# Optimization experiments

Measured on AMD Instinct MI355X. Metric: run time of the kernel, lower is better.

## Reference

```python
import jax, jax.numpy as jnp
import numpy as np
import math

B, C, IMG, P = 256, 3, 32, 4
D, H = 256, 8
HD = D // H
T = (IMG // P) ** 2          # 64 patches
T1 = T + 1                   # +cls token
MLP_H = 2048
HEAD_H = T * D // 2          # 8192
NUM_CLASSES = 10
PATCH_DIM = C * P * P


def _pe(t1, d):
    pos = jnp.arange(t1, dtype=jnp.float32)[:, None]
    div = jnp.exp(jnp.arange(0, d, 2, dtype=jnp.float32) * (-math.log(10000.0) / d))
    s = jnp.sin(pos * div)   # [T1, d/2]
    c = jnp.cos(pos * div)
    return jnp.stack([s, c], axis=-1).reshape(t1, d)  # interleave: even=sin, odd=cos


def _ln2d(x, w, b, eps=1e-5):
    # LayerNorm over last two dims [T1, D] with affine params of shape [T1, D]
    mu = jnp.mean(x, axis=(-2, -1), keepdims=True)
    var = jnp.mean((x - mu) ** 2, axis=(-2, -1), keepdims=True)
    return (x - mu) * jax.lax.rsqrt(var + eps) * w + b


def setup_inputs() -> dict:
    key = jax.random.key(0)
    ks = jax.random.split(key, 16)
    s = 0.02
    inp = {
        "x": jax.random.normal(ks[0], (B, C, IMG, IMG), dtype=jnp.float32),
        "cls_token": jax.random.normal(ks[1], (1, 1, D), dtype=jnp.float32),
        "Wp": jax.random.normal(ks[2], (PATCH_DIM, D), dtype=jnp.float32) * s,
        "bp": jnp.zeros((D,), jnp.float32),
        # 2 transformer blocks, params stacked on leading axis
        "qkv_w": jax.random.normal(ks[3], (2, D, 3 * D), dtype=jnp.float32) * s,
        "qkv_b": jnp.zeros((2, 3 * D), jnp.float32),
        "ln_w": jnp.ones((2, T1, D), jnp.float32),
        "ln_b": jnp.zeros((2, T1, D), jnp.float32),
        "mlp1_w": jax.random.normal(ks[4], (2, D, MLP_H), dtype=jnp.float32) * s,
        "mlp1_b": jnp.zeros((2, MLP_H), jnp.float32),
        "mlp2_w": jax.random.normal(ks[5], (2, MLP_H, D), dtype=jnp.float32) * s,
        "mlp2_b": jnp.zeros((2, D), jnp.float32),
        "head1_w": jax.random.normal(ks[6], (T1 * D, HEAD_H), dtype=jnp.float32) * s,
        "head1_b": jnp.zeros((HEAD_H,), jnp.float32),
        "head2_w": jax.random.normal(ks[7], (HEAD_H, NUM_CLASSES), dtype=jnp.float32) * s,
        "head2_b": jnp.zeros((NUM_CLASSES,), jnp.float32),
    }
    return inp


def reference(x, cls_token, Wp, bp, qkv_w, qkv_b, ln_w, ln_b,
              mlp1_w, mlp1_b, mlp2_w, mlp2_b, head1_w, head1_b, head2_w, head2_b):
    b = x.shape[0]
    n = IMG // P
    # patchify: [B,C,n,P,n,P] -> [B,n,n,C,P,P] -> [B, T, C*P*P]  (C-major per patch)
    patches = x.reshape(b, C, n, P, n, P).transpose(0, 2, 4, 1, 3, 5).reshape(b, T, PATCH_DIM)
    out = patches @ Wp + bp                                     # [B, T, D]
    cls = jnp.broadcast_to(cls_token, (b, 1, D))
    out = jnp.concatenate([cls, out], axis=1)                   # [B, T1, D]
    out = out + _pe(T1, D)[None]

    scale = 1.0 / math.sqrt(HD)
    for i in range(2):  # dropout is eval-mode identity
        h = _ln2d(out, ln_w[i], ln_b[i])
        qkv = (h @ qkv_w[i] + qkv_b[i]).reshape(b, T1, H, 3, HD)
        q, k, v = qkv[..., 0, :], qkv[..., 1, :], qkv[..., 2, :]   # [B,S,H,hd]
        scores = jnp.einsum('bqhd,bkhd->bhqk', q, k) * scale
        a = jax.nn.softmax(scores, axis=-1)
        attn = jnp.einsum('bhqk,bkhd->bqhd', a, v).reshape(b, T1, D)
        r = attn + out
        h2 = _ln2d(r, ln_w[i], ln_b[i])                          # same LN reused
        m = jax.nn.relu(h2 @ mlp1_w[i] + mlp1_b[i])
        out = (m @ mlp2_w[i] + mlp2_b[i]) + r

    flat = out.reshape(b, T1 * D)
    hidden = jax.nn.silu(flat @ head1_w + head1_b)
    return hidden @ head2_w + head2_b                            # [B, 10] logits
```

## Files before the change

kernel.cpp:

```cpp
#include <hip/hip_runtime.h>
#include <hip/hip_fp16.h>
#include <math.h>
#include <stdint.h>

#define B_ 256
#define C_ 3
#define IMG_ 32
#define D_ 256
#define H_ 8
#define HD_ 32
#define T1_ 65
#define MLP_H_ 2048
#define HEAD_H_ 8192
#define NCLS 10
#define PDIM 48
#define M_ROWS (B_*T1_)

typedef _Float16 f16;
typedef _Float16 f16x8 __attribute__((ext_vector_type(8)));
typedef _Float16 f16x4 __attribute__((ext_vector_type(4)));
typedef float f32x4 __attribute__((ext_vector_type(4)));

typedef const void __attribute__((address_space(1))) glob_cv;
typedef void __attribute__((address_space(3))) lds_v;

__device__ __forceinline__ void async16(const void* g, void* l) {
    __builtin_amdgcn_global_load_lds((glob_cv*)g, (lds_v*)l, 16, 0, 0);
}

__global__ __launch_bounds__(256) void patch_embed_kernel(
        const float* __restrict__ x, const float* __restrict__ cls,
        const float* __restrict__ Wp, const float* __restrict__ bp,
        float* __restrict__ out) {
    int bt = blockIdx.x;
    int b = bt / T1_;
    int t = bt % T1_;
    int d = threadIdx.x;
    int i2 = d & ~1;
    float div = expf((float)i2 * (-9.210340371976184f / 256.0f));
    float ang = (float)t * div;
    float pe = (d & 1) ? cosf(ang) : sinf(ang);

    __shared__ float patch[PDIM];
    if (t > 0) {
        int p = t - 1;
        int py = p >> 3, px = p & 7;
        if (threadIdx.x < PDIM) {
            int j = threadIdx.x;
            int c = j >> 4, r = j & 15;
            int iy = r >> 2, ix = r & 3;
            patch[j] = x[((b * C_ + c) * IMG_ + py * 4 + iy) * IMG_ + px * 4 + ix];
        }
    }
    __syncthreads();
    float acc;
    if (t == 0) {
        acc = cls[d];
    } else {
        acc = bp[d];
        #pragma unroll
        for (int j = 0; j < PDIM; ++j) acc += patch[j] * Wp[j * D_ + d];
    }
    out[(size_t)bt * D_ + d] = acc + pe;
}

__global__ __launch_bounds__(256) void ln_kernel(
        const float* __restrict__ xin, const float* __restrict__ w,
        const float* __restrict__ bb, f16* __restrict__ hout) {
    int b = blockIdx.x;
    const float* xb = xin + (size_t)b * (T1_ * D_);
    float s = 0.f, s2 = 0.f;
    for (int i = threadIdx.x; i < T1_ * D_; i += 256) {
        float v = xb[i]; s += v; s2 += v * v;
    }
    #pragma unroll
    for (int o = 32; o > 0; o >>= 1) { s += __shfl_down(s, o); s2 += __shfl_down(s2, o); }
    __shared__ float rs[4], rs2[4];
    __shared__ float mu_s, rstd_s;
    int wid = threadIdx.x >> 6;
    if ((threadIdx.x & 63) == 0) { rs[wid] = s; rs2[wid] = s2; }
    __syncthreads();
    if (threadIdx.x == 0) {
        float S = rs[0] + rs[1] + rs[2] + rs[3];
        float S2 = rs2[0] + rs2[1] + rs2[2] + rs2[3];
        const float inv_n = 1.0f / (float)(T1_ * D_);
        float mu = S * inv_n;
        float var = S2 * inv_n - mu * mu;
        mu_s = mu; rstd_s = rsqrtf(var + 1e-5f);
    }
    __syncthreads();
    float mu = mu_s, rstd = rstd_s;
    f16* hb = hout + (size_t)b * (T1_ * D_);
    for (int i = threadIdx.x; i < T1_ * D_; i += 256) {
        float v = (xb[i] - mu) * rstd * w[i] + bb[i];
        hb[i] = (f16)v;
    }
}

__global__ __launch_bounds__(256) void transpose_cvt(
        const float* __restrict__ W, f16* __restrict__ Wt, int K, int N) {
    __shared__ float L[32][33];
    int n0 = blockIdx.x * 32, k0 = blockIdx.y * 32;
    int t = threadIdx.x;
    int r = t >> 3, c4 = (t & 7) * 4;
    const float4 v = *(const float4*)(W + (size_t)(k0 + r) * N + n0 + c4);
    L[r][c4] = v.x; L[r][c4 + 1] = v.y; L[r][c4 + 2] = v.z; L[r][c4 + 3] = v.w;
    __syncthreads();
    f16x4 h;
    h[0] = (f16)L[c4][r]; h[1] = (f16)L[c4 + 1][r];
    h[2] = (f16)L[c4 + 2][r]; h[3] = (f16)L[c4 + 3][r];
    *(f16x4*)(Wt + (size_t)(n0 + r) * K + k0 + c4) = h;
}

template<int EPI, typename OutT>
__global__ __launch_bounds__(256) void gemm_f16(
        const f16* __restrict__ A, const f16* __restrict__ Bt,
        const float* __restrict__ bias, const float* __restrict__ Res,
        OutT* __restrict__ Cc, int M, int N, int K) {
    __shared__ __align__(16) f16 As[128 * 32];
    __shared__ __align__(16) f16 Bs[128 * 32];
    int nb = blockIdx.x, mb = blockIdx.y;
    int t = threadIdx.x;
    int lane = t & 63, wid = t >> 6;
    int wr = wid >> 1, wc = wid & 1;
    int lr = lane & 15, kq = lane >> 4;
    int row0 = mb * 128, col0 = nb * 128;

    f32x4 acc[4][4];
    #pragma unroll
    for (int mi = 0; mi < 4; ++mi)
        #pragma unroll
        for (int ni = 0; ni < 4; ++ni)
            #pragma unroll
            for (int r = 0; r < 4; ++r) acc[mi][ni][r] = 0.f;

    int sr = t >> 2;
    int k8 = (t & 3) * 8;
    const f16* Ab = A + (size_t)row0 * K + k8;
    const f16* Bb = Bt + (size_t)col0 * K + k8;

    for (int k0 = 0; k0 < K; k0 += 32) {
        __syncthreads();
        async16(Ab + (size_t)sr * K + k0,        &As[t * 8]);
        async16(Ab + (size_t)(sr + 64) * K + k0, &As[2048 + t * 8]);
        async16(Bb + (size_t)sr * K + k0,        &Bs[t * 8]);
        async16(Bb + (size_t)(sr + 64) * K + k0, &Bs[2048 + t * 8]);
        __syncthreads();
        f16x8 af[4], bf[4];
        #pragma unroll
        for (int mi = 0; mi < 4; ++mi)
            af[mi] = *(const f16x8*)&As[(wr * 64 + mi * 16 + lr) * 32 + kq * 8];
        #pragma unroll
        for (int ni = 0; ni < 4; ++ni)
            bf[ni] = *(const f16x8*)&Bs[(wc * 64 + ni * 16 + lr) * 32 + kq * 8];
        #pragma unroll
        for (int mi = 0; mi < 4; ++mi)
            #pragma unroll
            for (int ni = 0; ni < 4; ++ni)
                acc[mi][ni] = __builtin_amdgcn_mfma_f32_16x16x32_f16(af[mi], bf[ni], acc[mi][ni], 0, 0, 0);
    }

    #pragma unroll
    for (int mi = 0; mi < 4; ++mi) {
        #pragma unroll
        for (int ni = 0; ni < 4; ++ni) {
            int col = col0 + wc * 64 + ni * 16 + lr;
            #pragma unroll
            for (int r = 0; r < 4; ++r) {
                int row = row0 + wr * 64 + mi * 16 + kq * 4 + r;
                float v = acc[mi][ni][r] + bias[col];
                if (EPI == 1) v = fmaxf(v, 0.f);
                if (EPI == 2) v += Res[(size_t)row * N + col];
                Cc[(size_t)row * N + col] = (OutT)v;
            }
        }
    }
}

__global__ __launch_bounds__(256) void gemm_head1(
        const f16* __restrict__ A, const float* __restrict__ Bw,
        float* __restrict__ Cp) {
    __shared__ __align__(16) f16 As[256 * 32];
    __shared__ __align__(16) float Bs[32 * 64];
    const int K = M_ROWS, N = HEAD_H_;
    int nb = blockIdx.x;
    int z = blockIdx.y;
    int t = threadIdx.x;
    int lane = t & 63, wid = t >> 6;
    int lr = lane & 15, kq = lane >> 4;
    int col0 = nb * 64;
    int kstart = z * (K / 4);

    f32x4 acc[4][4];
    #pragma unroll
    for (int mi = 0; mi < 4; ++mi)
        #pragma unroll
        for (int ni = 0; ni < 4; ++ni)
            #pragma unroll
            for (int r = 0; r < 4; ++r) acc[mi][ni][r] = 0.f;

    int sr = t >> 2;
    int k8 = (t & 3) * 8;
    const f16* Ab = A + k8;
    int bkr = t >> 4;
    int bnc = (t & 15) * 4;
    const float* Bb = Bw + col0 + bnc;

    for (int k0 = kstart; k0 < kstart + K / 4; k0 += 32) {
        __syncthreads();
        #pragma unroll
        for (int r = 0; r < 4; ++r)
            async16(Ab + (size_t)(sr + r * 64) * K + k0, &As[r * 2048 + t * 8]);
        async16(Bb + (size_t)(k0 + bkr) * N,      &Bs[t * 4]);
        async16(Bb + (size_t)(k0 + 16 + bkr) * N, &Bs[1024 + t * 4]);
        __syncthreads();
        f16x8 af[4];
        #pragma unroll
        for (int mi = 0; mi < 4; ++mi)
            af[mi] = *(const f16x8*)&As[(wid * 64 + mi * 16 + lr) * 32 + kq * 8];
        #pragma unroll
        for (int ni = 0; ni < 4; ++ni) {
            f16x8 bf;
            #pragma unroll
            for (int j = 0; j < 8; ++j) bf[j] = (f16)Bs[(kq * 8 + j) * 64 + ni * 16 + lr];
            #pragma unroll
            for (int mi = 0; mi < 4; ++mi)
                acc[mi][ni] = __builtin_amdgcn_mfma_f32_16x16x32_f16(af[mi], bf, acc[mi][ni], 0, 0, 0);
        }
    }

    float* Cout = Cp + (size_t)z * 256 * N;
    #pragma unroll
    for (int mi = 0; mi < 4; ++mi) {
        #pragma unroll
        for (int ni = 0; ni < 4; ++ni) {
            int col = col0 + ni * 16 + lr;
            #pragma unroll
            for (int r = 0; r < 4; ++r) {
                int row = wid * 64 + mi * 16 + kq * 4 + r;
                Cout[(size_t)row * N + col] = acc[mi][ni][r];
            }
        }
    }
}

__global__ __launch_bounds__(256) void attn_kernel(
        const float* __restrict__ qkv, const float* __restrict__ outres,
        float* __restrict__ r) {
    int bh = blockIdx.x;
    int b = bh >> 3, h = bh & 7;
    __shared__ float q[T1_][HD_], k[T1_][HD_], v[T1_][HD_];
    __shared__ float s[T1_][T1_ + 1];
    const float* base = qkv + (size_t)b * T1_ * 768 + h * 96;
    for (int idx = threadIdx.x; idx < T1_ * 96; idx += 256) {
        int t = idx / 96, rem = idx % 96;
        int j = rem >> 5, d = rem & 31;
        float val = base[(size_t)t * 768 + rem];
        if (j == 0) q[t][d] = val; else if (j == 1) k[t][d] = val; else v[t][d] = val;
    }
    __syncthreads();
    const float scale = 0.17677669529663687f;
    for (int idx = threadIdx.x; idx < T1_ * T1_; idx += 256) {
        int qt = idx / T1_, kt = idx % T1_;
        float acc = 0.f;
        #pragma unroll
        for (int d = 0; d < HD_; ++d) acc += q[qt][d] * k[kt][d];
        s[qt][kt] = acc * scale;
    }
    __syncthreads();
    if (threadIdx.x < T1_) {
        int qt = threadIdx.x;
        float m = -1e30f;
        for (int kt = 0; kt < T1_; ++kt) m = fmaxf(m, s[qt][kt]);
        float sum = 0.f;
        for (int kt = 0; kt < T1_; ++kt) { float e = __expf(s[qt][kt] - m); s[qt][kt] = e; sum += e; }
        float inv = 1.f / sum;
        for (int kt = 0; kt < T1_; ++kt) s[qt][kt] *= inv;
    }
    __syncthreads();
    for (int idx = threadIdx.x; idx < T1_ * HD_; idx += 256) {
        int t = idx >> 5, d = idx & 31;
        float acc = 0.f;
        for (int kt = 0; kt < T1_; ++kt) acc += s[t][kt] * v[kt][d];
        size_t o = (size_t)(b * T1_ + t) * D_ + h * HD_ + d;
        r[o] = acc + outres[o];
    }
}

__global__ __launch_bounds__(256) void cvt_kernel(const float* __restrict__ in,
                                                  f16* __restrict__ o, int n) {
    int i = blockIdx.x * 256 + threadIdx.x;
    int stride = gridDim.x * 256;
    for (; i < n; i += stride) o[i] = (f16)in[i];
}

__global__ __launch_bounds__(256) void combine_silu(const float* __restrict__ part,
                                                    const float* __restrict__ bias,
                                                    float* __restrict__ o) {
    int idx = blockIdx.x * 256 + threadIdx.x;
    const int NP = 256 * HEAD_H_;
    float v = part[idx] + part[idx + NP] + part[idx + 2 * NP] + part[idx + 3 * NP]
            + bias[idx & (HEAD_H_ - 1)];
    o[idx] = v / (1.f + expf(-v));
}

__global__ __launch_bounds__(256) void head2_kernel(
        const float* __restrict__ hidden, const float* __restrict__ w,
        const float* __restrict__ bias, float* __restrict__ out) {
    int b = blockIdx.x;
    const float* hb = hidden + (size_t)b * HEAD_H_;
    float acc[NCLS];
    #pragma unroll
    for (int n = 0; n < NCLS; ++n) acc[n] = 0.f;
    for (int kk = threadIdx.x; kk < HEAD_H_; kk += 256) {
        float hv = hb[kk];
        const float* wr = w + (size_t)kk * NCLS;
        #pragma unroll
        for (int n = 0; n < NCLS; ++n) acc[n] += hv * wr[n];
    }
    #pragma unroll
    for (int n = 0; n < NCLS; ++n)
        #pragma unroll
        for (int o = 32; o > 0; o >>= 1) acc[n] += __shfl_down(acc[n], o);
    __shared__ float red[4][NCLS];
    int wid = threadIdx.x >> 6;
    if ((threadIdx.x & 63) == 0)
        for (int n = 0; n < NCLS; ++n) red[wid][n] = acc[n];
    __syncthreads();
    if (threadIdx.x < NCLS) {
        int n = threadIdx.x;
        out[(size_t)b * NCLS + n] = red[0][n] + red[1][n] + red[2][n] + red[3][n] + bias[n];
    }
}

extern "C" void kernel_launch(void* const* d_in, const int* in_sizes, int n_in,
                              void* d_out, int out_size, void* d_ws, size_t ws_size,
                              hipStream_t stream) {
    (void)in_sizes; (void)n_in; (void)out_size; (void)ws_size;
    const float* x       = (const float*)d_in[0];
    const float* cls     = (const float*)d_in[1];
    const float* Wp      = (const float*)d_in[2];
    const float* bp      = (const float*)d_in[3];
    const float* qkv_w   = (const float*)d_in[4];
    const float* qkv_b   = (const float*)d_in[5];
    const float* ln_w    = (const float*)d_in[6];
    const float* ln_b    = (const float*)d_in[7];
    const float* mlp1_w  = (const float*)d_in[8];
    const float* mlp1_b  = (const float*)d_in[9];
    const float* mlp2_w  = (const float*)d_in[10];
    const float* mlp2_b  = (const float*)d_in[11];
    const float* head1_w = (const float*)d_in[12];
    const float* head1_b = (const float*)d_in[13];
    const float* head2_w = (const float*)d_in[14];
    const float* head2_b = (const float*)d_in[15];
    float* outp = (float*)d_out;

    char* ws = (char*)d_ws;
    size_t off = 0;
    auto alloc = [&](size_t bytes) -> void* {
        void* p = ws + off; off += (bytes + 255) & ~(size_t)255; return p;
    };
    float* s_out = (float*)alloc((size_t)M_ROWS * D_ * 4);
    float* s_r   = (float*)alloc((size_t)M_ROWS * D_ * 4);
    f16*   s_h   = (f16*)  alloc((size_t)M_ROWS * D_ * 2);
    void*  s_big = alloc((size_t)M_ROWS * MLP_H_ * 2);
    f16*   w_qkv_t  = (f16*)alloc((size_t)2 * 768 * 256 * 2);
    f16*   w_mlp1_t = (f16*)alloc((size_t)2 * 2048 * 256 * 2);
    f16*   w_mlp2_t = (f16*)alloc((size_t)2 * 256 * 2048 * 2);
    f16*   s_flat   = s_h;
    float* s_hidden = s_out;
    float* s_qkv = (float*)s_big;
    f16*   s_m   = (f16*)s_big;
    float* s_part = (float*)s_big;

    dim3 blk(256);

    for (int i = 0; i < 2; ++i) {
        transpose_cvt<<<dim3(768 / 32, 256 / 32), blk, 0, stream>>>(
            qkv_w + (size_t)i * D_ * 768, w_qkv_t + (size_t)i * 768 * 256, 256, 768);
        transpose_cvt<<<dim3(2048 / 32, 256 / 32), blk, 0, stream>>>(
            mlp1_w + (size_t)i * D_ * 2048, w_mlp1_t + (size_t)i * 2048 * 256, 256, 2048);
        transpose_cvt<<<dim3(256 / 32, 2048 / 32), blk, 0, stream>>>(
            mlp2_w + (size_t)i * 2048 * 256, w_mlp2_t + (size_t)i * 256 * 2048, 2048, 256);
    }

    patch_embed_kernel<<<dim3(M_ROWS), blk, 0, stream>>>(x, cls, Wp, bp, s_out);

    for (int i = 0; i < 2; ++i) {
        const float* lw = ln_w + (size_t)i * T1_ * D_;
        const float* lb = ln_b + (size_t)i * T1_ * D_;
        ln_kernel<<<dim3(B_), blk, 0, stream>>>(s_out, lw, lb, s_h);
        gemm_f16<0, float><<<dim3(768 / 128, M_ROWS / 128), blk, 0, stream>>>(
            s_h, w_qkv_t + (size_t)i * 768 * 256, qkv_b + (size_t)i * 768,
            nullptr, s_qkv, M_ROWS, 768, 256);
        attn_kernel<<<dim3(B_ * H_), blk, 0, stream>>>(s_qkv, s_out, s_r);
        ln_kernel<<<dim3(B_), blk, 0, stream>>>(s_r, lw, lb, s_h);
        gemm_f16<1, f16><<<dim3(MLP_H_ / 128, M_ROWS / 128), blk, 0, stream>>>(
            s_h, w_mlp1_t + (size_t)i * 2048 * 256, mlp1_b + (size_t)i * MLP_H_,
            nullptr, s_m, M_ROWS, MLP_H_, 256);
        gemm_f16<2, float><<<dim3(D_ / 128, M_ROWS / 128), blk, 0, stream>>>(
            s_m, w_mlp2_t + (size_t)i * 256 * 2048, mlp2_b + (size_t)i * D_,
            s_r, s_out, M_ROWS, D_, MLP_H_);
    }

    cvt_kernel<<<dim3(1024), blk, 0, stream>>>(s_out, s_flat, M_ROWS * D_);
    gemm_head1<<<dim3(HEAD_H_ / 64, 4), blk, 0, stream>>>(s_flat, head1_w, s_part);
    combine_silu<<<dim3(B_ * HEAD_H_ / 256), blk, 0, stream>>>(s_part, head1_b, s_hidden);
    head2_kernel<<<dim3(B_), blk, 0, stream>>>(s_hidden, head2_w, head2_b, outp);
}
```

Measured before the change: 1.376 ms.

## Move patch embed and attention to MFMA, fuse small kernels, use fp16 qkv

Rewrites patch embedding as a per-image MFMA GEMM against a pre-transposed fp16 weight, and rewrites attention to use MFMA for QK^T and PV with fp16 Q/K/V stored in LDS. The QKV projection now writes fp16, and LayerNorm uses float4 loads with 1024-thread blocks. The final MLP2 GEMM also emits the fp16 flattened copy, which removes the separate convert kernel. The split-K combine plus SiLU is fused into the head2 reduction. The goal is to cut the many small, memory-bound kernels and the scalar FP32 attention math, at the cost of extra fp16 rounding in the attention inputs and probabilities.

Result: faster. 1.169 ms (-15.0%).

```diff
diff --git a/kernel.cpp b/kernel.cpp
--- a/kernel.cpp
+++ b/kernel.cpp
@@ -28,61 +28,90 @@
     __builtin_amdgcn_global_load_lds((glob_cv*)g, (lds_v*)l, 16, 0, 0);
 }
 
-__global__ __launch_bounds__(256) void patch_embed_kernel(
+__global__ __launch_bounds__(256) void wpt_build(const float* __restrict__ Wp,
+                                                 f16* __restrict__ WpT) {
+    int idx = blockIdx.x * 256 + threadIdx.x;
+    int d = idx >> 6, j = idx & 63;
+    WpT[idx] = (j < PDIM) ? (f16)Wp[j * D_ + d] : (f16)0.f;
+}
+
+__global__ __launch_bounds__(256) void patch_mfma(
         const float* __restrict__ x, const float* __restrict__ cls,
-        const float* __restrict__ Wp, const float* __restrict__ bp,
+        const f16* __restrict__ WpT, const float* __restrict__ bp,
         float* __restrict__ out) {
-    int bt = blockIdx.x;
-    int b = bt / T1_;
-    int t = bt % T1_;
-    int d = threadIdx.x;
-    int i2 = d & ~1;
-    float div = expf((float)i2 * (-9.210340371976184f / 256.0f));
-    float ang = (float)t * div;
-    float pe = (d & 1) ? cosf(ang) : sinf(ang);
-
-    __shared__ float patch[PDIM];
-    if (t > 0) {
-        int p = t - 1;
-        int py = p >> 3, px = p & 7;
-        if (threadIdx.x < PDIM) {
-            int j = threadIdx.x;
-            int c = j >> 4, r = j & 15;
-            int iy = r >> 2, ix = r & 3;
-            patch[j] = x[((b * C_ + c) * IMG_ + py * 4 + iy) * IMG_ + px * 4 + ix];
-        }
-    }
-    __syncthreads();
-    float acc;
-    if (t == 0) {
-        acc = cls[d];
-    } else {
-        acc = bp[d];
-        #pragma unroll
-        for (int j = 0; j < PDIM; ++j) acc += patch[j] * Wp[j * D_ + d];
-    }
-    out[(size_t)bt * D_ + d] = acc + pe;
-}
-
-__global__ __launch_bounds__(256) void ln_kernel(
+    int b = blockIdx.x;
+    __shared__ float xs[3072];
+    __shared__ __align__(16) f16 Ap[64 * 64];
+    __shared__ __align__(16) f16 Bp[256 * 64];
+    int tid = threadIdx.x;
+    int lane = tid & 63, wid = tid >> 6;
+    int lr = lane & 15, kq = lane >> 4;
+
+    for (int i = tid; i < 768; i += 256)
+        ((float4*)xs)[i] = ((const float4*)(x + (size_t)b * 3072))[i];
+    for (int i = tid; i < 2048; i += 256)
+        async16(WpT + (size_t)i * 8, &Bp[i * 8]);
+    __syncthreads();
+    for (int i = tid; i < 64 * 64; i += 256) {
+        int t = i >> 6, j = i & 63;
+        float val = 0.f;
+        if (j < PDIM) {
+            int py = t >> 3, px = t & 7;
+            int c = j >> 4, rr = j & 15;
+            int iy = rr >> 2, ix = rr & 3;
+            val = xs[c * 1024 + (py * 4 + iy) * 32 + px * 4 + ix];
+        }
+        Ap[i] = (f16)val;
+    }
+    __syncthreads();
+
+    for (int tile = wid; tile < 64; tile += 4) {
+        int mi = tile >> 4, ni = tile & 15;
+        f32x4 acc = {0.f, 0.f, 0.f, 0.f};
+        #pragma unroll
+        for (int ks = 0; ks < 2; ++ks) {
+            f16x8 a = *(const f16x8*)&Ap[(mi * 16 + lr) * 64 + ks * 32 + kq * 8];
+            f16x8 bb = *(const f16x8*)&Bp[(ni * 16 + lr) * 64 + ks * 32 + kq * 8];
+            acc = __builtin_amdgcn_mfma_f32_16x16x32_f16(a, bb, acc, 0, 0, 0);
+        }
+        int d = ni * 16 + lr;
+        float div = __expf((float)(d & ~1) * (-9.210340371976184f / 256.0f));
+        #pragma unroll
+        for (int r = 0; r < 4; ++r) {
+            int t = 1 + mi * 16 + kq * 4 + r;
+            float ang = (float)t * div;
+            float pe = (d & 1) ? __cosf(ang) : __sinf(ang);
+            out[((size_t)b * T1_ + t) * D_ + d] = acc[r] + bp[d] + pe;
+        }
+    }
+    out[(size_t)b * T1_ * D_ + tid] = cls[tid] + ((tid & 1) ? 1.f : 0.f);
+}
+
+__global__ __launch_bounds__(1024) void ln_kernel(
         const float* __restrict__ xin, const float* __restrict__ w,
         const float* __restrict__ bb, f16* __restrict__ hout) {
     int b = blockIdx.x;
-    const float* xb = xin + (size_t)b * (T1_ * D_);
+    const float4* x4 = (const float4*)(xin + (size_t)b * (T1_ * D_));
+    const float4* w4 = (const float4*)w;
+    const float4* b4 = (const float4*)bb;
+    int tid = threadIdx.x;
     float s = 0.f, s2 = 0.f;
-    for (int i = threadIdx.x; i < T1_ * D_; i += 256) {
-        float v = xb[i]; s += v; s2 += v * v;
+    for (int i = tid; i < 4160; i += 1024) {
+        float4 v = x4[i];
+        s  += v.x + v.y + v.z + v.w;
+        s2 += v.x * v.x + v.y * v.y + v.z * v.z + v.w * v.w;
     }
     #pragma unroll
     for (int o = 32; o > 0; o >>= 1) { s += __shfl_down(s, o); s2 += __shfl_down(s2, o); }
-    __shared__ float rs[4], rs2[4];
+    __shared__ float rs[16], rs2[16];
     __shared__ float mu_s, rstd_s;
-    int wid = threadIdx.x >> 6;
-    if ((threadIdx.x & 63) == 0) { rs[wid] = s; rs2[wid] = s2; }
-    __syncthreads();
-    if (threadIdx.x == 0) {
-        float S = rs[0] + rs[1] + rs[2] + rs[3];
-        float S2 = rs2[0] + rs2[1] + rs2[2] + rs2[3];
+    int wid = tid >> 6;
+    if ((tid & 63) == 0) { rs[wid] = s; rs2[wid] = s2; }
+    __syncthreads();
+    if (tid == 0) {
+        float S = 0.f, S2 = 0.f;
+        #pragma unroll
+        for (int i = 0; i < 16; ++i) { S += rs[i]; S2 += rs2[i]; }
         const float inv_n = 1.0f / (float)(T1_ * D_);
         float mu = S * inv_n;
         float var = S2 * inv_n - mu * mu;
@@ -91,9 +120,14 @@
     __syncthreads();
     float mu = mu_s, rstd = rstd_s;
     f16* hb = hout + (size_t)b * (T1_ * D_);
-    for (int i = threadIdx.x; i < T1_ * D_; i += 256) {
-        float v = (xb[i] - mu) * rstd * w[i] + bb[i];
-        hb[i] = (f16)v;
+    for (int i = tid; i < 4160; i += 1024) {
+        float4 v = x4[i]; float4 wv = w4[i]; float4 bv = b4[i];
+        f16x4 h;
+        h[0] = (f16)((v.x - mu) * rstd * wv.x + bv.x);
+        h[1] = (f16)((v.y - mu) * rstd * wv.y + bv.y);
+        h[2] = (f16)((v.z - mu) * rstd * wv.z + bv.z);
+        h[3] = (f16)((v.w - mu) * rstd * wv.w + bv.w);
+        *(f16x4*)(hb + i * 4) = h;
     }
 }
 
@@ -116,7 +150,7 @@
 __global__ __launch_bounds__(256) void gemm_f16(
         const f16* __restrict__ A, const f16* __restrict__ Bt,
         const float* __restrict__ bias, const float* __restrict__ Res,
-        OutT* __restrict__ Cc, int M, int N, int K) {
+        OutT* __restrict__ Cc, f16* __restrict__ C2, int M, int N, int K) {
     __shared__ __align__(16) f16 As[128 * 32];
     __shared__ __align__(16) f16 Bs[128 * 32];
     int nb = blockIdx.x, mb = blockIdx.y;
@@ -170,8 +204,9 @@
                 int row = row0 + wr * 64 + mi * 16 + kq * 4 + r;
                 float v = acc[mi][ni][r] + bias[col];
                 if (EPI == 1) v = fmaxf(v, 0.f);
-                if (EPI == 2) v += Res[(size_t)row * N + col];
+                if (EPI == 2 || EPI == 3) v += Res[(size_t)row * N + col];
                 Cc[(size_t)row * N + col] = (OutT)v;
+                if (EPI == 3) C2[(size_t)row * N + col] = (f16)v;
             }
         }
     }
@@ -245,91 +280,126 @@
 }
 
 __global__ __launch_bounds__(256) void attn_kernel(
-        const float* __restrict__ qkv, const float* __restrict__ outres,
+        const f16* __restrict__ qkv, const float* __restrict__ outres,
         float* __restrict__ r) {
-    int bh = blockIdx.x;
-    int b = bh >> 3, h = bh & 7;
-    __shared__ float q[T1_][HD_], k[T1_][HD_], v[T1_][HD_];
-    __shared__ float s[T1_][T1_ + 1];
-    const float* base = qkv + (size_t)b * T1_ * 768 + h * 96;
-    for (int idx = threadIdx.x; idx < T1_ * 96; idx += 256) {
-        int t = idx / 96, rem = idx % 96;
-        int j = rem >> 5, d = rem & 31;
-        float val = base[(size_t)t * 768 + rem];
-        if (j == 0) q[t][d] = val; else if (j == 1) k[t][d] = val; else v[t][d] = val;
-    }
-    __syncthreads();
+    int b = blockIdx.x >> 3, h = blockIdx.x & 7;
+    __shared__ __align__(16) f16 Qs[80 * 32];
+    __shared__ __align__(16) f16 Ks[80 * 32];
+    __shared__ __align__(16) f16 Vt[32 * 96];
+    __shared__ float Sf[80 * 81];
+    __shared__ __align__(16) f16 Pf[80 * 96];
+    int tid = threadIdx.x;
+    int lane = tid & 63, wid = tid >> 6;
+    int lr = lane & 15, kq = lane >> 4;
     const float scale = 0.17677669529663687f;
-    for (int idx = threadIdx.x; idx < T1_ * T1_; idx += 256) {
-        int qt = idx / T1_, kt = idx % T1_;
-        float acc = 0.f;
-        #pragma unroll
-        for (int d = 0; d < HD_; ++d) acc += q[qt][d] * k[kt][d];
-        s[qt][kt] = acc * scale;
-    }
-    __syncthreads();
-    if (threadIdx.x < T1_) {
-        int qt = threadIdx.x;
+
+    const f16* base = qkv + (size_t)b * T1_ * 768 + h * 96;
+    for (int i = tid; i < T1_ * 12; i += 256) {
+        int t = i / 12, c = i % 12;
+        f16x8 vv = *(const f16x8*)(base + (size_t)t * 768 + c * 8);
+        if (c < 4) {
+            f16x8 q8;
+            #pragma unroll
+            for (int j = 0; j < 8; ++j) q8[j] = (f16)((float)vv[j] * scale);
+            *(f16x8*)&Qs[t * 32 + c * 8] = q8;
+        } else if (c < 8) {
+            *(f16x8*)&Ks[t * 32 + (c - 4) * 8] = vv;
+        } else {
+            int d0 = (c - 8) * 8;
+            #pragma unroll
+            for (int j = 0; j < 8; ++j) Vt[(d0 + j) * 96 + t] = vv[j];
+        }
+    }
+    for (int i = tid; i < 32 * 31; i += 256) {
+        int d = i / 31, kt = 65 + i % 31;
+        Vt[d * 96 + kt] = (f16)0.f;
+    }
+    __syncthreads();
+
+    for (int tile = wid; tile < 25; tile += 4) {
+        int mi = tile / 5, ni = tile % 5;
+        f16x8 a = *(const f16x8*)&Qs[(mi * 16 + lr) * 32 + kq * 8];
+        f16x8 bb = *(const f16x8*)&Ks[(ni * 16 + lr) * 32 + kq * 8];
+        f32x4 c = {0.f, 0.f, 0.f, 0.f};
+        c = __builtin_amdgcn_mfma_f32_16x16x32_f16(a, bb, c, 0, 0, 0);
+        #pragma unroll
+        for (int rr2 = 0; rr2 < 4; ++rr2)
+            Sf[(mi * 16 + kq * 4 + rr2) * 81 + ni * 16 + lr] = c[rr2];
+    }
+    __syncthreads();
+
+    for (int row = tid >> 2; row < T1_; row += 64) {
+        int sub = tid & 3;
         float m = -1e30f;
-        for (int kt = 0; kt < T1_; ++kt) m = fmaxf(m, s[qt][kt]);
+        for (int kt = sub; kt < T1_; kt += 4) m = fmaxf(m, Sf[row * 81 + kt]);
+        m = fmaxf(m, __shfl_xor(m, 1));
+        m = fmaxf(m, __shfl_xor(m, 2));
         float sum = 0.f;
-        for (int kt = 0; kt < T1_; ++kt) { float e = __expf(s[qt][kt] - m); s[qt][kt] = e; sum += e; }
+        for (int kt = sub; kt < T1_; kt += 4) {
+            float e = __expf(Sf[row * 81 + kt] - m);
+            Sf[row * 81 + kt] = e; sum += e;
+        }
+        sum += __shfl_xor(sum, 1);
+        sum += __shfl_xor(sum, 2);
         float inv = 1.f / sum;
-        for (int kt = 0; kt < T1_; ++kt) s[qt][kt] *= inv;
-    }
-    __syncthreads();
-    for (int idx = threadIdx.x; idx < T1_ * HD_; idx += 256) {
-        int t = idx >> 5, d = idx & 31;
-        float acc = 0.f;
-        for (int kt = 0; kt < T1_; ++kt) acc += s[t][kt] * v[kt][d];
-        size_t o = (size_t)(b * T1_ + t) * D_ + h * HD_ + d;
-        r[o] = acc + outres[o];
-    }
-}
-
-__global__ __launch_bounds__(256) void cvt_kernel(const float* __restrict__ in,
-                                                  f16* __restrict__ o, int n) {
-    int i = blockIdx.x * 256 + threadIdx.x;
-    int stride = gridDim.x * 256;
-    for (; i < n; i += stride) o[i] = (f16)in[i];
-}
-
-__global__ __launch_bounds__(256) void combine_silu(const float* __restrict__ part,
-                                                    const float* __restrict__ bias,
-                                                    float* __restrict__ o) {
-    int idx = blockIdx.x * 256 + threadIdx.x;
+        for (int kt = sub; kt < T1_; kt += 4)
+            Pf[row * 96 + kt] = (f16)(Sf[row * 81 + kt] * inv);
+        for (int kt = T1_ + sub; kt < 96; kt += 4)
+            Pf[row * 96 + kt] = (f16)0.f;
+    }
+    __syncthreads();
+
+    for (int tile = wid; tile < 10; tile += 4) {
+        int mi = tile >> 1, ni = tile & 1;
+        f32x4 acc = {0.f, 0.f, 0.f, 0.f};
+        #pragma unroll
+        for (int ks = 0; ks < 3; ++ks) {
+            f16x8 a = *(const f16x8*)&Pf[(mi * 16 + lr) * 96 + ks * 32 + kq * 8];
+            f16x8 bv = *(const f16x8*)&Vt[(ni * 16 + lr) * 96 + ks * 32 + kq * 8];
+            acc = __builtin_amdgcn_mfma_f32_16x16x32_f16(a, bv, acc, 0, 0, 0);
+        }
+        #pragma unroll
+        for (int rr2 = 0; rr2 < 4; ++rr2) {
+            int qt = mi * 16 + kq * 4 + rr2;
+            if (qt < T1_) {
+                size_t o = ((size_t)b * T1_ + qt) * D_ + h * HD_ + ni * 16 + lr;
+                r[o] = acc[rr2] + outres[o];
+            }
+        }
+    }
+}
+
+__global__ __launch_bounds__(256) void head2_fused(
+        const float* __restrict__ part, const float* __restrict__ h1b,
+        const float* __restrict__ w, const float* __restrict__ h2b,
+        float* __restrict__ out) {
+    int b = blockIdx.x;
     const int NP = 256 * HEAD_H_;
-    float v = part[idx] + part[idx + NP] + part[idx + 2 * NP] + part[idx + 3 * NP]
-            + bias[idx & (HEAD_H_ - 1)];
-    o[idx] = v / (1.f + expf(-v));
-}
-
-__global__ __launch_bounds__(256) void head2_kernel(
-        const float* __restrict__ hidden, const float* __restrict__ w,
-        const float* __restrict__ bias, float* __restrict__ out) {
-    int b = blockIdx.x;
-    const float* hb = hidden + (size_t)b * HEAD_H_;
+    int tid = threadIdx.x;
     float acc[NCLS];
     #pragma unroll
     for (int n = 0; n < NCLS; ++n) acc[n] = 0.f;
-    for (int kk = threadIdx.x; kk < HEAD_H_; kk += 256) {
-        float hv = hb[kk];
+    for (int kk = tid; kk < HEAD_H_; kk += 256) {
+        size_t o = (size_t)b * HEAD_H_ + kk;
+        float v = part[o] + part[o + NP] + part[o + 2 * (size_t)NP] + part[o + 3 * (size_t)NP]
+                + h1b[kk];
+        v = v / (1.f + __expf(-v));
         const float* wr = w + (size_t)kk * NCLS;
         #pragma unroll
-        for (int n = 0; n < NCLS; ++n) acc[n] += hv * wr[n];
+        for (int n = 0; n < NCLS; ++n) acc[n] += v * wr[n];
     }
     #pragma unroll
     for (int n = 0; n < NCLS; ++n)
         #pragma unroll
         for (int o = 32; o > 0; o >>= 1) acc[n] += __shfl_down(acc[n], o);
     __shared__ float red[4][NCLS];
-    int wid = threadIdx.x >> 6;
-    if ((threadIdx.x & 63) == 0)
+    int wid = tid >> 6;
+    if ((tid & 63) == 0)
         for (int n = 0; n < NCLS; ++n) red[wid][n] = acc[n];
     __syncthreads();
-    if (threadIdx.x < NCLS) {
-        int n = threadIdx.x;
-        out[(size_t)b * NCLS + n] = red[0][n] + red[1][n] + red[2][n] + red[3][n] + bias[n];
+    if (tid < NCLS) {
+        int n = tid;
+        out[(size_t)b * NCLS + n] = red[0][n] + red[1][n] + red[2][n] + red[3][n] + h2b[n];
     }
 }
 
@@ -367,9 +437,9 @@
     f16*   w_qkv_t  = (f16*)alloc((size_t)2 * 768 * 256 * 2);
     f16*   w_mlp1_t = (f16*)alloc((size_t)2 * 2048 * 256 * 2);
     f16*   w_mlp2_t = (f16*)alloc((size_t)2 * 256 * 2048 * 2);
+    f16*   wpT      = (f16*)alloc((size_t)256 * 64 * 2);
     f16*   s_flat   = s_h;
-    float* s_hidden = s_out;
-    float* s_qkv = (float*)s_big;
+    f16*   s_qkv = (f16*)s_big;
     f16*   s_m   = (f16*)s_big;
     float* s_part = (float*)s_big;
 
@@ -383,28 +453,32 @@
         transpose_cvt<<<dim3(256 / 32, 2048 / 32), blk, 0, stream>>>(
             mlp2_w + (size_t)i * 2048 * 256, w_mlp2_t + (size_t)i * 256 * 2048, 2048, 256);
     }
-
-    patch_embed_kernel<<<dim3(M_ROWS), blk, 0, stream>>>(x, cls, Wp, bp, s_out);
+    wpt_build<<<dim3(64), blk, 0, stream>>>(Wp, wpT);
+    patch_mfma<<<dim3(B_), blk, 0, stream>>>(x, cls, wpT, bp, s_out);
 
     for (int i = 0; i < 2; ++i) {
         const float* lw = ln_w + (size_t)i * T1_ * D_;
         const float* lb = ln_b + (size_t)i * T1_ * D_;
-        ln_kernel<<<dim3(B_), blk, 0, stream>>>(s_out, lw, lb, s_h);
-        gemm_f16<0, float><<<dim3(768 / 128, M_ROWS / 128), blk, 0, stream>>>(
+        ln_kernel<<<dim3(B_), dim3(1024), 0, stream>>>(s_out, lw, lb, s_h);
+        gemm_f16<0, f16><<<dim3(768 / 128, M_ROWS / 128), blk, 0, stream>>>(
             s_h, w_qkv_t + (size_t)i * 768 * 256, qkv_b + (size_t)i * 768,
-            nullptr, s_qkv, M_ROWS, 768, 256);
+            nullptr, s_qkv, nullptr, M_ROWS, 768, 256);
         attn_kernel<<<dim3(B_ * H_), blk, 0, stream>>>(s_qkv, s_out, s_r);
-        ln_kernel<<<dim3(B_), blk, 0, stream>>>(s_r, lw, lb, s_h);
+        ln_kernel<<<dim3(B_), dim3(1024), 0, stream>>>(s_r, lw, lb, s_h);
         gemm_f16<1, f16><<<dim3(MLP_H_ / 128, M_ROWS / 128), blk, 0, stream>>>(
             s_h, w_mlp1_t + (size_t)i * 2048 * 256, mlp1_b + (size_t)i * MLP_H_,
-            nullptr, s_m, M_ROWS, MLP_H_, 256);
-        gemm_f16<2, float><<<dim3(D_ / 128, M_ROWS / 128), blk, 0, stream>>>(
-            s_m, w_mlp2_t + (size_t)i * 256 * 2048, mlp2_b + (size_t)i * D_,
-            s_r, s_out, M_ROWS, D_, MLP_H_);
-    }
-
-    cvt_kernel<<<dim3(1024), blk, 0, stream>>>(s_out, s_flat, M_ROWS * D_);
+            nullptr, s_m, nullptr, M_ROWS, MLP_H_, 256);
+        if (i == 0) {
+            gemm_f16<2, float><<<dim3(D_ / 128, M_ROWS / 128), blk, 0, stream>>>(
+                s_m, w_mlp2_t + (size_t)i * 256 * 2048, mlp2_b + (size_t)i * D_,
+                s_r, s_out, nullptr, M_ROWS, D_, MLP_H_);
+        } else {
+            gemm_f16<3, float><<<dim3(D_ / 128, M_ROWS / 128), blk, 0, stream>>>(
+                s_m, w_mlp2_t + (size_t)i * 256 * 2048, mlp2_b + (size_t)i * D_,
+                s_r, s_out, s_flat, M_ROWS, D_, MLP_H_);
+        }
+    }
+
     gemm_head1<<<dim3(HEAD_H_ / 64, 4), blk, 0, stream>>>(s_flat, head1_w, s_part);
-    combine_silu<<<dim3(B_ * HEAD_H_ / 256), blk, 0, stream>>>(s_part, head1_b, s_hidden);
-    head2_kernel<<<dim3(B_), blk, 0, stream>>>(s_hidden, head2_w, head2_b, outp);
-}
+    head2_fused<<<dim3(B_), blk, 0, stream>>>(s_part, head1_b, head2_w, head2_b, outp);
+}
```
